# Kernel optimization log

Hardware: AMD Instinct MI355X
Metric: run time of the kernel (lower is better)

## Reference

```python
import jax, jax.numpy as jnp
import numpy as np

N_NODES = 8192
N_EDGES = 32768
D = 768
H1 = 8
NEG_SLOPE = 0.2


def setup_inputs() -> dict:
    key = jax.random.key(0)
    ks = jax.random.split(key, 10)
    s = 0.02  # init scale keeps attention logits numerically tame
    x = jax.random.normal(ks[0], (N_NODES, D), dtype=jnp.float32)
    edge_index = jax.random.randint(ks[1], (2, N_EDGES), 0, N_NODES, dtype=jnp.int64)
    W1 = jax.random.normal(ks[2], (D, H1 * D), dtype=jnp.float32) * s
    a_src1 = jax.random.normal(ks[3], (H1, D), dtype=jnp.float32) * s
    a_dst1 = jax.random.normal(ks[4], (H1, D), dtype=jnp.float32) * s
    b1 = jnp.zeros((H1 * D,), dtype=jnp.float32)
    W2 = jax.random.normal(ks[5], (H1 * D, D), dtype=jnp.float32) * s
    a_src2 = jax.random.normal(ks[6], (1, D), dtype=jnp.float32) * s
    a_dst2 = jax.random.normal(ks[7], (1, D), dtype=jnp.float32) * s
    b2 = jnp.zeros((D,), dtype=jnp.float32)
    return {"x": x, "edge_index": edge_index, "W1": W1, "a_src1": a_src1,
            "a_dst1": a_dst1, "b1": b1, "W2": W2, "a_src2": a_src2,
            "a_dst2": a_dst2, "b2": b2}


def gat_conv(x, src, dst, W, a_src, a_dst, b, heads, out_ch):
    """PyG GATConv (concat=True, self-loops already appended to src/dst)."""
    n = x.shape[0]
    h = (x @ W).reshape(n, heads, out_ch)            # [N,H,C]
    alpha_src = jnp.einsum("nhc,hc->nh", h, a_src)  # [N,H]
    alpha_dst = jnp.einsum("nhc,hc->nh", h, a_dst)  # [N,H]
    # edge scores: leaky_relu(a_src.h_j + a_dst.h_i) for edge j->i
    e = jax.nn.leaky_relu(alpha_src[src] + alpha_dst[dst], NEG_SLOPE)  # [E,H]
    # segment softmax over incoming edges of each destination node
    m = jax.ops.segment_max(e, dst, num_segments=n)   # [N,H]
    m = jnp.where(jnp.isfinite(m), m, 0.0)
    p = jnp.exp(e - m[dst])                           # [E,H]
    denom = jax.ops.segment_sum(p, dst, num_segments=n)
    alpha = p / denom[dst]                            # [E,H]
    msg = h[src] * alpha[:, :, None]                  # [E,H,C] gather+weight
    out = jax.ops.segment_sum(msg, dst, num_segments=n)  # [N,H,C] scatter-add
    return out.reshape(n, heads * out_ch) + b


def reference(x, edge_index, W1, a_src1, a_dst1, b1, W2, a_src2, a_dst2, b2):
    n = x.shape[0]
    loops = jnp.arange(n, dtype=edge_index.dtype)
    src = jnp.concatenate([edge_index[0], loops])  # add_self_loops=True
    dst = jnp.concatenate([edge_index[1], loops])
    h = gat_conv(x, src, dst, W1, a_src1, a_dst1, b1, H1, D)
    h = jax.nn.elu(h)
    out = gat_conv(h, src, dst, W2, a_src2, a_dst2, b2, 1, D)
    return out
```

## Files before the change

kernel.cpp:

```cpp
#include <hip/hip_runtime.h>
#include <hip/hip_bf16.h>


#define N_NODES 8192
#define N_EDGES 32768
#define E_TOT   (N_EDGES + N_NODES)
#define D_IN    768
#define H1      8
#define HC1     (H1 * D_IN)
#define KSPLIT  4
#define KSLICE  (HC1 / KSPLIT)

typedef unsigned short ushort_t;
using short8  = __attribute__((ext_vector_type(8))) short;
using floatx4 = __attribute__((ext_vector_type(4))) float;

__device__ __forceinline__ float bf2f(unsigned short u) {
  return __uint_as_float(((unsigned)u) << 16);
}
__device__ __forceinline__ unsigned short f2bf(float f) {
  unsigned u = __float_as_uint(f);
  unsigned r = (u + 0x7fffu + ((u >> 16) & 1u)) >> 16;
  return (unsigned short)r;
}

__device__ __forceinline__ void gll16(const ushort_t* g, ushort_t* l) {
  __builtin_amdgcn_global_load_lds(
      (const __attribute__((address_space(1))) void*)g,
      (__attribute__((address_space(3))) void*)l, 16, 0, 0);
}

__global__ __launch_bounds__(64) void frag_transpose_kernel(
    const float* __restrict__ W, ushort_t* __restrict__ out,
    int Kdim, int Ndim) {
  const int bn = blockIdx.x;
  const int bk = blockIdx.y;
  const int lane = threadIdx.x;
  const int lrow = lane & 15, lq = lane >> 4;
  const int n = bn * 16 + lrow;
  const int kb = bk * 32 + lq * 8;
  ushort_t v[8];
#pragma unroll
  for (int e = 0; e < 8; ++e)
    v[e] = f2bf(W[(size_t)(kb + e) * Ndim + n]);
  *(short8*)(out + ((size_t)bn * (Kdim >> 5) + bk) * 512 + lane * 8) =
      *(short8*)v;
}

__global__ void prep_aw_kernel(const float* __restrict__ W1,
                               const float* __restrict__ aS,
                               const float* __restrict__ aD,
                               float* __restrict__ awS,
                               float* __restrict__ awD) {
  const int d = blockIdx.x;
  const int t = threadIdx.x;
  const float* row = W1 + (size_t)d * HC1;
  float ps[H1], pd[H1];
#pragma unroll
  for (int h = 0; h < H1; ++h) { ps[h] = 0.f; pd[h] = 0.f; }
#pragma unroll
  for (int h = 0; h < H1; ++h)
#pragma unroll
    for (int j = 0; j < 3; ++j) {
      int idx = h * 768 + j * 256 + t;
      float w = row[idx];
      ps[h] += w * aS[idx];
      pd[h] += w * aD[idx];
    }
#pragma unroll
  for (int h = 0; h < H1; ++h)
    for (int off = 32; off > 0; off >>= 1) {
      ps[h] += __shfl_down(ps[h], off, 64);
      pd[h] += __shfl_down(pd[h], off, 64);
    }
  __shared__ float red[2][4][H1];
  int w = t >> 6;
  if ((t & 63) == 0) {
#pragma unroll
    for (int h = 0; h < H1; ++h) { red[0][w][h] = ps[h]; red[1][w][h] = pd[h]; }
  }
  __syncthreads();
  if (t < H1)
    awS[d * H1 + t] = red[0][0][t] + red[0][1][t] + red[0][2][t] + red[0][3][t];
  else if (t >= 64 && t < 64 + H1) {
    int h = t - 64;
    awD[d * H1 + h] = red[1][0][h] + red[1][1][h] + red[1][2][h] + red[1][3][h];
  }
}

__global__ void node_prep_kernel(const float* __restrict__ x,
                                 const float* __restrict__ awS,
                                 const float* __restrict__ awD,
                                 ushort_t* __restrict__ xb,
                                 float* __restrict__ as1,
                                 float* __restrict__ ad1) {
  const int n = blockIdx.x;
  const int t = threadIdx.x;
  float ps[H1], pd[H1];
#pragma unroll
  for (int h = 0; h < H1; ++h) { ps[h] = 0.f; pd[h] = 0.f; }
#pragma unroll
  for (int j = 0; j < 3; ++j) {
    int d = j * 256 + t;
    float xv = x[(size_t)n * 768 + d];
    xb[(size_t)n * 768 + d] = f2bf(xv);
    const float4* s4 = (const float4*)(awS + d * 8);
    const float4* d4 = (const float4*)(awD + d * 8);
    float4 a0 = s4[0], a1 = s4[1];
    float4 c0 = d4[0], c1 = d4[1];
    ps[0] += xv * a0.x; ps[1] += xv * a0.y; ps[2] += xv * a0.z; ps[3] += xv * a0.w;
    ps[4] += xv * a1.x; ps[5] += xv * a1.y; ps[6] += xv * a1.z; ps[7] += xv * a1.w;
    pd[0] += xv * c0.x; pd[1] += xv * c0.y; pd[2] += xv * c0.z; pd[3] += xv * c0.w;
    pd[4] += xv * c1.x; pd[5] += xv * c1.y; pd[6] += xv * c1.z; pd[7] += xv * c1.w;
  }
#pragma unroll
  for (int h = 0; h < H1; ++h)
    for (int off = 32; off > 0; off >>= 1) {
      ps[h] += __shfl_down(ps[h], off, 64);
      pd[h] += __shfl_down(pd[h], off, 64);
    }
  __shared__ float red[2][4][H1];
  int w = t >> 6;
  if ((t & 63) == 0) {
#pragma unroll
    for (int h = 0; h < H1; ++h) { red[0][w][h] = ps[h]; red[1][w][h] = pd[h]; }
  }
  __syncthreads();
  if (t < H1)
    as1[n * H1 + t] = red[0][0][t] + red[0][1][t] + red[0][2][t] + red[0][3][t];
  else if (t >= 64 && t < 64 + H1) {
    int h = t - 64;
    ad1[n * H1 + h] = red[1][0][h] + red[1][1][h] + red[1][2][h] + red[1][3][h];
  }
}

__global__ void deg_kernel(const int* __restrict__ dst, int* __restrict__ deg) {
  int e = blockIdx.x * blockDim.x + threadIdx.x;
  if (e >= E_TOT) return;
  int d = (e < N_EDGES) ? dst[e] : (e - N_EDGES);
  atomicAdd(&deg[d], 1);
}

__global__ void scan_kernel(const int* __restrict__ deg, int* __restrict__ start,
                            int* __restrict__ cursor) {
  __shared__ int sums[1024];
  int t = threadIdx.x;
  int base = t * 8;
  int local[8];
  int s = 0;
#pragma unroll
  for (int i = 0; i < 8; ++i) { local[i] = s; s += deg[base + i]; }
  sums[t] = s;
  __syncthreads();
  for (int off = 1; off < 1024; off <<= 1) {
    int v = (t >= off) ? sums[t - off] : 0;
    __syncthreads();
    sums[t] += v;
    __syncthreads();
  }
  int excl = (t == 0) ? 0 : sums[t - 1];
#pragma unroll
  for (int i = 0; i < 8; ++i) {
    int st = excl + local[i];
    start[base + i] = st;
    cursor[base + i] = st;
  }
}

__global__ void fill_kernel(const int* __restrict__ dst, int* __restrict__ cursor,
                            int* __restrict__ csr) {
  int e = blockIdx.x * blockDim.x + threadIdx.x;
  if (e >= E_TOT) return;
  int d = (e < N_EDGES) ? dst[e] : (e - N_EDGES);
  int pos = atomicAdd(&cursor[d], 1);
  csr[pos] = e;
}

__global__ __launch_bounds__(256) void attn1_kernel(
    const ushort_t* __restrict__ xb, const float* __restrict__ as1,
    const float* __restrict__ ad1, const int* __restrict__ start,
    const int* __restrict__ deg, const int* __restrict__ csr,
    const int* __restrict__ src, ushort_t* __restrict__ z_sw) {
  const int n = blockIdx.x;
  const int t = threadIdx.x;
  const int st = start[n], dg = deg[n];
  const int h = t & 7, eloc = t >> 3;
  __shared__ float invd[H1];
  __shared__ float alphaS[16][H1];
  __shared__ int sidx[16];
  __shared__ float red[4][H1];
  __shared__ uint4 xs[16 * 96];

  const float adv = ad1[n * H1 + h];
  float pden = 0.f;
  for (int base = 0; base < dg; base += 32) {
    int ei = base + eloc;
    if (ei < dg) {
      int e = csr[st + ei];
      int s = (e < N_EDGES) ? src[e] : (e - N_EDGES);
      float l = as1[s * H1 + h] + adv;
      l = l > 0.f ? l : 0.2f * l;
      pden += __expf(l);
    }
  }
  pden += __shfl_down(pden, 8, 64);
  pden += __shfl_down(pden, 16, 64);
  pden += __shfl_down(pden, 32, 64);
  if ((t & 63) < 8) red[t >> 6][h] = pden;
  __syncthreads();
  if (t < 8) invd[t] = 1.0f / (red[0][t] + red[1][t] + red[2][t] + red[3][t]);
  __syncthreads();

  int hp[3], ip[3];
#pragma unroll
  for (int p = 0; p < 3; ++p) {
    int c8 = p * 256 + t;
    hp[p] = c8 / 96;
    ip[p] = c8 % 96;
  }
  float acc[3][8];
#pragma unroll
  for (int p = 0; p < 3; ++p)
#pragma unroll
    for (int e = 0; e < 8; ++e) acc[p][e] = 0.f;

  for (int base = 0; base < dg; base += 16) {
    int cnt = dg - base; if (cnt > 16) cnt = 16;
    if (t < 128 && eloc < cnt) {
      int e = csr[st + base + eloc];
      int s = (e < N_EDGES) ? src[e] : (e - N_EDGES);
      float l = as1[s * H1 + h] + adv;
      l = l > 0.f ? l : 0.2f * l;
      alphaS[eloc][h] = __expf(l) * invd[h];
      if (h == 0) sidx[eloc] = s;
    }
    __syncthreads();
#pragma unroll
    for (int j = 0; j < 6; ++j) {
      int idx = t + 256 * j;
      int row = idx / 96;
      if (row < cnt) {
        int col = idx - row * 96;
        xs[idx] = *(const uint4*)(xb + (size_t)sidx[row] * 768 + col * 8);
      }
    }
    __syncthreads();
    for (int ei = 0; ei < cnt; ++ei) {
      const uint4* xr = &xs[ei * 96];
#pragma unroll
      for (int p = 0; p < 3; ++p) {
        uint4 v = xr[ip[p]];
        float al = alphaS[ei][hp[p]];
        unsigned uu[4] = {v.x, v.y, v.z, v.w};
#pragma unroll
        for (int q = 0; q < 4; ++q) {
          acc[p][2 * q]     += al * __uint_as_float(uu[q] << 16);
          acc[p][2 * q + 1] += al * __uint_as_float(uu[q] & 0xffff0000u);
        }
      }
    }
    __syncthreads();
  }
#pragma unroll
  for (int p = 0; p < 3; ++p) {
    int c8 = p * 256 + t;
    int k = c8 * 8;
    size_t chunk = (size_t)(n >> 4) * 192 + (k >> 5);
    int word = ((k >> 3) & 3) * 16 + (n & 15);
    ushort_t v[8];
#pragma unroll
    for (int e = 0; e < 8; ++e) v[e] = f2bf(acc[p][e]);
    *(short8*)(z_sw + chunk * 512 + word * 8) = *(short8*)v;
  }
}

#define STAGE_RING(t)                                                          \
  {                                                                            \
    ushort_t* ld_ = smem + ((t) & 3) * 16384 + slot512;                        \
    _Pragma("unroll") for (int q_ = 0; q_ < 4; ++q_)                           \
        gll16(SRC + (((size_t)(cb[q_] + (t))) << 9) + lane8, ld_ + q_ * 512);  \
  }

#define GSTEP_BODY(s, VMSTR, NSV)                                             \
  {                                                                           \
    asm volatile("s_waitcnt vmcnt(" VMSTR ")" ::: "memory");                  \
    __builtin_amdgcn_s_barrier();                                             \
    const ushort_t* buf_ = smem + ((s) & 3) * 16384;                          \
    short8 af[8], bf[4];                                                      \
    _Pragma("unroll") for (int j_ = 0; j_ < 4; ++j_)                          \
        bf[j_] = *(const short8*)(buf_ + 8192 + (wn * 4 + j_) * 512 + lane8); \
    _Pragma("unroll") for (int i_ = 0; i_ < 4; ++i_)                          \
        af[i_] = *(const short8*)(buf_ + (wm * 8 + i_) * 512 + lane8);        \
    if ((s) + 3 < (NSV)) STAGE_RING((s) + 3)                                  \
    __builtin_amdgcn_s_setprio(1);                                            \
    _Pragma("unroll") for (int i_ = 0; i_ < 4; ++i_)                          \
        _Pragma("unroll") for (int j_ = 0; j_ < 4; ++j_)                      \
            acc[i_][j_] = __builtin_amdgcn_mfma_f32_16x16x32_bf16(            \
                af[i_], bf[j_], acc[i_][j_], 0, 0, 0);                        \
    __builtin_amdgcn_s_setprio(0);                                            \
    _Pragma("unroll") for (int i_ = 4; i_ < 8; ++i_)                          \
        af[i_] = *(const short8*)(buf_ + (wm * 8 + i_) * 512 + lane8);        \
    __builtin_amdgcn_s_barrier();                                             \
    __builtin_amdgcn_s_setprio(1);                                            \
    _Pragma("unroll") for (int i_ = 4; i_ < 8; ++i_)                          \
        _Pragma("unroll") for (int j_ = 0; j_ < 4; ++j_)                      \
            acc[i_][j_] = __builtin_amdgcn_mfma_f32_16x16x32_bf16(            \
                af[i_], bf[j_], acc[i_][j_], 0, 0, 0);                        \
    __builtin_amdgcn_s_setprio(0);                                            \
  }

#define GEMM_PIPE(NSV)                                                        \
  _Pragma("unroll") for (int p_ = 0; p_ < 3; ++p_) STAGE_RING(p_)             \
  _Pragma("unroll 2") for (int s_ = 0; s_ < (NSV)-2; ++s_) {                  \
    GSTEP_BODY(s_, "8", (NSV))                                                \
  }                                                                           \
  GSTEP_BODY((NSV)-2, "4", (NSV))                                             \
  GSTEP_BODY((NSV)-1, "0", (NSV))

__global__ __launch_bounds__(512, 2) void gemm_l1_kernel(
    const ushort_t* __restrict__ Asw, const ushort_t* __restrict__ Bsw,
    const float* __restrict__ biasb, ushort_t* __restrict__ Csw) {
  __shared__ ushort_t smem[4 * 16384];
  const int id = blockIdx.x;
  const int head = id & 7;
  const int j_id = id >> 3;
  const int n_t = j_id % 3;
  const int m_t = j_id / 3;
  const int tid = threadIdx.x;
  const int lane = tid & 63;
  const int w = tid >> 6;
  const int wm = w >> 2, wn = w & 3;
  const int lrow = lane & 15, lq = lane >> 4;
  const int lane8 = lane * 8;
  const int slot512 = w * 2048;
  const ushort_t* SRC = (w < 4) ? Asw : Bsw;

  int cb[4];
#pragma unroll
  for (int q = 0; q < 4; ++q) {
    int v;
    if (w < 4)
      v = (m_t * 16 + 4 * w + q) * 192 + head * 24;
    else
      v = (head * 48 + n_t * 16 + 4 * (w - 4) + q) * 24;
    cb[q] = __builtin_amdgcn_readfirstlane(v);
  }

  floatx4 acc[8][4];
#pragma unroll
  for (int i = 0; i < 8; ++i)
#pragma unroll
    for (int j = 0; j < 4; ++j) acc[i][j] = {0.f, 0.f, 0.f, 0.f};

  GEMM_PIPE(24)

  __syncthreads();
  ushort_t* tile = smem;
  const float* bias = biasb + head * 768 + n_t * 256;
#pragma unroll
  for (int p = 0; p < 2; ++p) {
    if (p) __syncthreads();
    if (wm == p) {
#pragma unroll
      for (int i = 0; i < 8; ++i)
#pragma unroll
        for (int j = 0; j < 4; ++j) {
          int col = wn * 64 + j * 16 + lrow;
          float bv = bias[col];
#pragma unroll
          for (int r = 0; r < 4; ++r) {
            float v = acc[i][j][r] + bv;
            v = v > 0.f ? v : __expf(v) - 1.0f;
            tile[(i * 16 + lq * 4 + r) * 280 + col] = f2bf(v);
          }
        }
    }
    __syncthreads();
#pragma unroll
    for (int cc = 0; cc < 8; ++cc) {
      int ch = w * 8 + cc;
      int RB = ch >> 3, kg = ch & 7;
      short8 vv =
          *(const short8*)&tile[(RB * 16 + lrow) * 280 + kg * 32 + lq * 8];
      size_t chunk_g = (size_t)(m_t * 16 + p * 8 + RB) * 192 + head * 24 +
                       n_t * 8 + kg;
      *((short8*)Csw + chunk_g * 64 + lane) = vv;
    }
  }
}

__global__ __launch_bounds__(512, 2) void gemm_l2_kernel(
    const ushort_t* __restrict__ Asw, const ushort_t* __restrict__ Bsw,
    float* __restrict__ Cp) {
  __shared__ ushort_t smem[4 * 16384];
  const int id = blockIdx.x;
  const int c = id & 7;
  const int sl = c >> 1;
  const int j_id = id >> 3;
  const int n_t = j_id % 3;
  const int m_t = (j_id / 3) * 2 + (c & 1);
  const int tid = threadIdx.x;
  const int lane = tid & 63;
  const int w = tid >> 6;
  const int wm = w >> 2, wn = w & 3;
  const int lrow = lane & 15, lq = lane >> 4;
  const int lane8 = lane * 8;
  const int slot512 = w * 2048;
  const ushort_t* SRC = (w < 4) ? Asw : Bsw;

  int cb[4];
#pragma unroll
  for (int q = 0; q < 4; ++q) {
    int v;
    if (w < 4)
      v = (m_t * 16 + 4 * w + q) * 192 + sl * 48;
    else
      v = (n_t * 16 + 4 * (w - 4) + q) * 192 + sl * 48;
    cb[q] = __builtin_amdgcn_readfirstlane(v);
  }

  floatx4 acc[8][4];
#pragma unroll
  for (int i = 0; i < 8; ++i)
#pragma unroll
    for (int j = 0; j < 4; ++j) acc[i][j] = {0.f, 0.f, 0.f, 0.f};

  GEMM_PIPE(48)

  float* C = Cp + (size_t)sl * N_NODES * 768;
  const int m0 = m_t * 256, n0 = n_t * 256;
#pragma unroll
  for (int i = 0; i < 8; ++i) {
    int row_b = m0 + wm * 128 + i * 16 + lq * 4;
#pragma unroll
    for (int j = 0; j < 4; ++j) {
      int col = n0 + wn * 64 + j * 16 + lrow;
#pragma unroll
      for (int r = 0; r < 4; ++r)
        C[(size_t)(row_b + r) * 768 + col] = acc[i][j][r];
    }
  }
}

__global__ void reduce_alpha2_kernel(const float* __restrict__ parts,
                                     const float* __restrict__ aS,
                                     const float* __restrict__ aD,
                                     ushort_t* __restrict__ yb,
                                     float* __restrict__ as2,
                                     float* __restrict__ ad2) {
  const int n = blockIdx.x;
  const int t = threadIdx.x;
  const size_t S = (size_t)N_NODES * 768;
  float ps = 0.f, pd = 0.f;
#pragma unroll
  for (int j = 0; j < 3; ++j) {
    int cidx = j * 256 + t;
    size_t base = (size_t)n * 768 + cidx;
    float v = parts[base] + parts[base + S] + parts[base + 2 * S] +
              parts[base + 3 * S];
    yb[base] = f2bf(v);
    ps += v * aS[cidx];
    pd += v * aD[cidx];
  }
  for (int off = 32; off > 0; off >>= 1) {
    ps += __shfl_down(ps, off, 64);
    pd += __shfl_down(pd, off, 64);
  }
  __shared__ float red[2][4];
  int w = t >> 6;
  if ((t & 63) == 0) { red[0][w] = ps; red[1][w] = pd; }
  __syncthreads();
  if (t == 0) as2[n] = red[0][0] + red[0][1] + red[0][2] + red[0][3];
  if (t == 64) ad2[n] = red[1][0] + red[1][1] + red[1][2] + red[1][3];
}

__global__ __launch_bounds__(256) void attn2_kernel(
    const ushort_t* __restrict__ yb, const float* __restrict__ as2,
    const float* __restrict__ ad2, const int* __restrict__ start,
    const int* __restrict__ deg, const int* __restrict__ csr,
    const int* __restrict__ src, const float* __restrict__ b2,
    float* __restrict__ out) {
  const int n = blockIdx.x;
  const int t = threadIdx.x;
  const int st = start[n], dg = deg[n];
  __shared__ float alphaS[64];
  __shared__ int sidx[64];
  __shared__ float red[4];
  __shared__ float invd_sh;

  const float adv = ad2[n];
  float pden = 0.f;
  for (int ei = t; ei < dg; ei += 256) {
    int e = csr[st + ei];
    int s = (e < N_EDGES) ? src[e] : (e - N_EDGES);
    float l = as2[s] + adv;
    l = l > 0.f ? l : 0.2f * l;
    pden += __expf(l);
  }
  for (int off = 32; off > 0; off >>= 1) pden += __shfl_down(pden, off, 64);
  if ((t & 63) == 0) red[t >> 6] = pden;
  __syncthreads();
  if (t == 0) invd_sh = 1.0f / (red[0] + red[1] + red[2] + red[3]);
  __syncthreads();
  const float invd = invd_sh;

  float a0 = 0.f, a1 = 0.f, a2 = 0.f;
  for (int base = 0; base < dg; base += 64) {
    int cnt = dg - base; if (cnt > 64) cnt = 64;
    if (t < cnt) {
      int e = csr[st + base + t];
      int s = (e < N_EDGES) ? src[e] : (e - N_EDGES);
      float l = as2[s] + adv;
      l = l > 0.f ? l : 0.2f * l;
      alphaS[t] = __expf(l) * invd;
      sidx[t] = s;
    }
    __syncthreads();
    for (int ei = 0; ei < cnt; ++ei) {
      float al = alphaS[ei];
      const ushort_t* row = yb + (size_t)sidx[ei] * 768;
      a0 += al * bf2f(row[t]);
      a1 += al * bf2f(row[t + 256]);
      a2 += al * bf2f(row[t + 512]);
    }
    __syncthreads();
  }
  out[(size_t)n * 768 + t]       = a0 + b2[t];
  out[(size_t)n * 768 + t + 256] = a1 + b2[t + 256];
  out[(size_t)n * 768 + t + 512] = a2 + b2[t + 512];
}

extern "C" void kernel_launch(void* const* d_in, const int* in_sizes, int n_in,
                              void* d_out, int out_size, void* d_ws, size_t ws_size,
                              hipStream_t stream) {
  const float* x      = (const float*)d_in[0];
  const int*   ei     = (const int*)d_in[1];
  const float* W1     = (const float*)d_in[2];
  const float* a_src1 = (const float*)d_in[3];
  const float* a_dst1 = (const float*)d_in[4];
  const float* b1     = (const float*)d_in[5];
  const float* W2     = (const float*)d_in[6];
  const float* a_src2 = (const float*)d_in[7];
  const float* a_dst2 = (const float*)d_in[8];
  const float* b2     = (const float*)d_in[9];
  float* out = (float*)d_out;
  const int* src = ei;
  const int* dst = ei + N_EDGES;

  char* ws = (char*)d_ws;
  size_t off = 0;
  auto alloc = [&](size_t bytes) -> void* {
    void* p = ws + off;
    off = (off + bytes + 255) & ~(size_t)255;
    return p;
  };

  int* deg = (int*)alloc(N_NODES * 4);
  float* awS = (float*)alloc(768 * H1 * 4);
  float* awD = (float*)alloc(768 * H1 * 4);
  float* as1 = (float*)alloc(N_NODES * H1 * 4);
  float* ad1 = (float*)alloc(N_NODES * H1 * 4);
  float* as2 = (float*)alloc(N_NODES * 4);
  float* ad2 = (float*)alloc(N_NODES * 4);
  int* start  = (int*)alloc(N_NODES * 4);
  int* cursor = (int*)alloc(N_NODES * 4);
  int* csr    = (int*)alloc(E_TOT * 4);
  ushort_t* xb     = (ushort_t*)alloc((size_t)N_NODES * D_IN * 2);
  ushort_t* w1t_sw = (ushort_t*)alloc((size_t)HC1 * D_IN * 2 + 8192);
  ushort_t* w2t_sw = (ushort_t*)alloc((size_t)HC1 * D_IN * 2 + 8192);
  ushort_t* z_sw   = (ushort_t*)alloc((size_t)N_NODES * HC1 * 2 + 8192);
  ushort_t* h2b_sw = (ushort_t*)alloc((size_t)N_NODES * HC1 * 2 + 8192);
  ushort_t* yb  = xb;
  float* parts  = (float*)z_sw;
  (void)ws_size; (void)n_in; (void)in_sizes; (void)out_size;

  hipMemsetAsync(deg, 0, N_NODES * 4, stream);

  prep_aw_kernel<<<768, 256, 0, stream>>>(W1, a_src1, a_dst1, awS, awD);
  node_prep_kernel<<<N_NODES, 256, 0, stream>>>(x, awS, awD, xb, as1, ad1);
  frag_transpose_kernel<<<dim3(HC1 / 16, D_IN / 32), 64, 0, stream>>>(
      W1, w1t_sw, D_IN, HC1);
  frag_transpose_kernel<<<dim3(D_IN / 16, HC1 / 32), 64, 0, stream>>>(
      W2, w2t_sw, HC1, D_IN);

  deg_kernel<<<(E_TOT + 255) / 256, 256, 0, stream>>>(dst, deg);
  scan_kernel<<<1, 1024, 0, stream>>>(deg, start, cursor);
  fill_kernel<<<(E_TOT + 255) / 256, 256, 0, stream>>>(dst, cursor, csr);

  attn1_kernel<<<N_NODES, 256, 0, stream>>>(xb, as1, ad1, start, deg, csr,
                                            src, z_sw);
  gemm_l1_kernel<<<8 * 32 * 3, 512, 0, stream>>>(z_sw, w1t_sw, b1, h2b_sw);

  gemm_l2_kernel<<<KSPLIT * 2 * 16 * 3, 512, 0, stream>>>(h2b_sw, w2t_sw,
                                                          parts);
  reduce_alpha2_kernel<<<N_NODES, 256, 0, stream>>>(parts, a_src2, a_dst2, yb,
                                                    as2, ad2);
  attn2_kernel<<<N_NODES, 256, 0, stream>>>(yb, as2, ad2, start, deg, csr,
                                            src, b2, out);
}
```

Baseline: 462.6 us.

## Replace 4-slot K-step ring with double-buffered two-step tiles in GEMMs

Both GEMM kernels move from a 4-deep ring of single K-steps, with prefetch three ahead and partial vmcnt waits, to a 2-buffer scheme. Each buffer holds two K-steps, and each iteration prefetches the next tile while computing the current one. Interleaved LDS reads and MFMA clusters are separated by barriers, explicit lgkmcnt waits and sched_barriers. The aim is fewer barrier/wait points per K and a simpler schedule. The cost is shallower prefetch, since a full vmcnt(0) wait happens every tile, and there are more barriers inside each tile.

```diff
diff --git a/kernel.cpp b/kernel.cpp
--- a/kernel.cpp
+++ b/kernel.cpp
@@ -274,53 +274,66 @@
   }
 }
 
-#define STAGE_RING(t)                                                          \
-  {                                                                            \
-    ushort_t* ld_ = smem + ((t) & 3) * 16384 + slot512;                        \
-    _Pragma("unroll") for (int q_ = 0; q_ < 4; ++q_)                           \
-        gll16(SRC + (((size_t)(cb[q_] + (t))) << 9) + lane8, ld_ + q_ * 512);  \
-  }
-
-#define GSTEP_BODY(s, VMSTR, NSV)                                             \
+#define STAGE_TILE(t)                                                         \
   {                                                                           \
-    asm volatile("s_waitcnt vmcnt(" VMSTR ")" ::: "memory");                  \
+    ushort_t* ld_ = smem + ((t) & 1) * 32768 + slotu;                         \
+    _Pragma("unroll") for (int kk_ = 0; kk_ < 2; ++kk_)                       \
+      _Pragma("unroll") for (int q_ = 0; q_ < 4; ++q_)                        \
+        gll16(SRC + (((size_t)(cb[q_] + 2 * (t) + kk_)) << 9) + lane8,        \
+              ld_ + kk_ * 16384 + q_ * 512);                                  \
+  }
+
+#define READS_A(tb_, kk)                                                      \
+    _Pragma("unroll") for (int j_ = 0; j_ < 4; ++j_)                          \
+      bf[j_] = *(const short8*)((tb_) + (kk) * 16384 + 8192 +                 \
+                                (wn * 4 + j_) * 512 + lane8);                 \
+    _Pragma("unroll") for (int i_ = 0; i_ < 4; ++i_)                          \
+      af[i_] = *(const short8*)((tb_) + (kk) * 16384 +                        \
+                                (wm * 8 + i_) * 512 + lane8);
+
+#define READS_B(tb_, kk)                                                      \
+    _Pragma("unroll") for (int i_ = 0; i_ < 4; ++i_)                          \
+      af2[i_] = *(const short8*)((tb_) + (kk) * 16384 +                       \
+                                 (wm * 8 + 4 + i_) * 512 + lane8);
+
+#define MFMA_CL(ab, FR)                                                       \
     __builtin_amdgcn_s_barrier();                                             \
-    const ushort_t* buf_ = smem + ((s) & 3) * 16384;                          \
-    short8 af[8], bf[4];                                                      \
-    _Pragma("unroll") for (int j_ = 0; j_ < 4; ++j_)                          \
-        bf[j_] = *(const short8*)(buf_ + 8192 + (wn * 4 + j_) * 512 + lane8); \
-    _Pragma("unroll") for (int i_ = 0; i_ < 4; ++i_)                          \
-        af[i_] = *(const short8*)(buf_ + (wm * 8 + i_) * 512 + lane8);        \
-    if ((s) + 3 < (NSV)) STAGE_RING((s) + 3)                                  \
+    asm volatile("s_waitcnt lgkmcnt(0)" ::: "memory");                        \
+    __builtin_amdgcn_sched_barrier(0);                                        \
     __builtin_amdgcn_s_setprio(1);                                            \
     _Pragma("unroll") for (int i_ = 0; i_ < 4; ++i_)                          \
-        _Pragma("unroll") for (int j_ = 0; j_ < 4; ++j_)                      \
-            acc[i_][j_] = __builtin_amdgcn_mfma_f32_16x16x32_bf16(            \
-                af[i_], bf[j_], acc[i_][j_], 0, 0, 0);                        \
-    __builtin_amdgcn_s_setprio(0);                                            \
-    _Pragma("unroll") for (int i_ = 4; i_ < 8; ++i_)                          \
-        af[i_] = *(const short8*)(buf_ + (wm * 8 + i_) * 512 + lane8);        \
+      _Pragma("unroll") for (int j_ = 0; j_ < 4; ++j_)                        \
+        acc[(ab) + i_][j_] = __builtin_amdgcn_mfma_f32_16x16x32_bf16(         \
+            FR[i_], bf[j_], acc[(ab) + i_][j_], 0, 0, 0);                     \
+    __builtin_amdgcn_s_setprio(0);
+
+#define GEMM_TILE8(t, NT)                                                     \
+  {                                                                           \
+    asm volatile("s_waitcnt vmcnt(0)" ::: "memory");                          \
     __builtin_amdgcn_s_barrier();                                             \
-    __builtin_amdgcn_s_setprio(1);                                            \
-    _Pragma("unroll") for (int i_ = 4; i_ < 8; ++i_)                          \
-        _Pragma("unroll") for (int j_ = 0; j_ < 4; ++j_)                      \
-            acc[i_][j_] = __builtin_amdgcn_mfma_f32_16x16x32_bf16(            \
-                af[i_], bf[j_], acc[i_][j_], 0, 0, 0);                        \
-    __builtin_amdgcn_s_setprio(0);                                            \
-  }
-
-#define GEMM_PIPE(NSV)                                                        \
-  _Pragma("unroll") for (int p_ = 0; p_ < 3; ++p_) STAGE_RING(p_)             \
-  _Pragma("unroll 2") for (int s_ = 0; s_ < (NSV)-2; ++s_) {                  \
-    GSTEP_BODY(s_, "8", (NSV))                                                \
-  }                                                                           \
-  GSTEP_BODY((NSV)-2, "4", (NSV))                                             \
-  GSTEP_BODY((NSV)-1, "0", (NSV))
+    if ((t) + 1 < (NT)) STAGE_TILE((t) + 1)                                   \
+    const ushort_t* tb_ = smem + ((t) & 1) * 32768;                           \
+    short8 af[4], af2[4], bf[4];                                              \
+    READS_A(tb_, 0)                                                           \
+    MFMA_CL(0, af)                                                            \
+    READS_B(tb_, 0)                                                           \
+    MFMA_CL(4, af2)                                                           \
+    READS_A(tb_, 1)                                                           \
+    MFMA_CL(0, af)                                                            \
+    READS_B(tb_, 1)                                                           \
+    MFMA_CL(4, af2)                                                           \
+  }
+
+#define GEMM_PIPE8(NT)                                                        \
+  STAGE_TILE(0)                                                               \
+  _Pragma("unroll 2") for (int t_ = 0; t_ < (NT); ++t_) {                     \
+    GEMM_TILE8(t_, (NT))                                                      \
+  }
 
 __global__ __launch_bounds__(512, 2) void gemm_l1_kernel(
     const ushort_t* __restrict__ Asw, const ushort_t* __restrict__ Bsw,
     const float* __restrict__ biasb, ushort_t* __restrict__ Csw) {
-  __shared__ ushort_t smem[4 * 16384];
+  __shared__ ushort_t smem[65536];
   const int id = blockIdx.x;
   const int head = id & 7;
   const int j_id = id >> 3;
@@ -332,7 +345,7 @@
   const int wm = w >> 2, wn = w & 3;
   const int lrow = lane & 15, lq = lane >> 4;
   const int lane8 = lane * 8;
-  const int slot512 = w * 2048;
+  const int slotu = (w < 4) ? w * 2048 : 8192 + (w - 4) * 2048;
   const ushort_t* SRC = (w < 4) ? Asw : Bsw;
 
   int cb[4];
@@ -352,7 +365,7 @@
 #pragma unroll
     for (int j = 0; j < 4; ++j) acc[i][j] = {0.f, 0.f, 0.f, 0.f};
 
-  GEMM_PIPE(24)
+  GEMM_PIPE8(12)
 
   __syncthreads();
   ushort_t* tile = smem;
@@ -392,7 +405,7 @@
 __global__ __launch_bounds__(512, 2) void gemm_l2_kernel(
     const ushort_t* __restrict__ Asw, const ushort_t* __restrict__ Bsw,
     float* __restrict__ Cp) {
-  __shared__ ushort_t smem[4 * 16384];
+  __shared__ ushort_t smem[65536];
   const int id = blockIdx.x;
   const int c = id & 7;
   const int sl = c >> 1;
@@ -405,7 +418,7 @@
   const int wm = w >> 2, wn = w & 3;
   const int lrow = lane & 15, lq = lane >> 4;
   const int lane8 = lane * 8;
-  const int slot512 = w * 2048;
+  const int slotu = (w < 4) ? w * 2048 : 8192 + (w - 4) * 2048;
   const ushort_t* SRC = (w < 4) ? Asw : Bsw;
 
   int cb[4];
@@ -425,7 +438,7 @@
 #pragma unroll
     for (int j = 0; j < 4; ++j) acc[i][j] = {0.f, 0.f, 0.f, 0.f};
 
-  GEMM_PIPE(48)
+  GEMM_PIPE8(24)
 
   float* C = Cp + (size_t)sl * N_NODES * 768;
   const int m0 = m_t * 256, n0 = n_t * 256;
```

Result: slower. 475.1 us (+2.7%).

## Fuse W1 attention-weight precompute into LDS-tiled bf16 fragment transpose

Applied to the files above, without the earlier changes.

The weight transpose kernels now stage a 64x64 fp32 tile in padded LDS so global reads are coalesced, then emit the bf16 MFMA fragment layout from shared memory. The separate prep_aw pass over W1 is folded into the W1 transpose. It reuses the staged tile to compute the per-head a_src/a_dst projections and accumulates them with atomics, so it needs two extra memsets. This drops a full re-read of W1 and the strided uncoalesced loads of the old transpose, at the cost of atomic float accumulation with nondeterministic summation order.

```diff
diff --git a/kernel.cpp b/kernel.cpp
--- a/kernel.cpp
+++ b/kernel.cpp
@@ -30,61 +30,84 @@
       (__attribute__((address_space(3))) void*)l, 16, 0, 0);
 }
 
-__global__ __launch_bounds__(64) void frag_transpose_kernel(
+__global__ __launch_bounds__(256) void frag_transpose_kernel(
     const float* __restrict__ W, ushort_t* __restrict__ out,
     int Kdim, int Ndim) {
-  const int bn = blockIdx.x;
-  const int bk = blockIdx.y;
-  const int lane = threadIdx.x;
-  const int lrow = lane & 15, lq = lane >> 4;
-  const int n = bn * 16 + lrow;
-  const int kb = bk * 32 + lq * 8;
-  ushort_t v[8];
-#pragma unroll
-  for (int e = 0; e < 8; ++e)
-    v[e] = f2bf(W[(size_t)(kb + e) * Ndim + n]);
-  *(short8*)(out + ((size_t)bn * (Kdim >> 5) + bk) * 512 + lane * 8) =
-      *(short8*)v;
-}
-
-__global__ void prep_aw_kernel(const float* __restrict__ W1,
-                               const float* __restrict__ aS,
-                               const float* __restrict__ aD,
-                               float* __restrict__ awS,
-                               float* __restrict__ awD) {
-  const int d = blockIdx.x;
-  const int t = threadIdx.x;
-  const float* row = W1 + (size_t)d * HC1;
-  float ps[H1], pd[H1];
-#pragma unroll
-  for (int h = 0; h < H1; ++h) { ps[h] = 0.f; pd[h] = 0.f; }
-#pragma unroll
-  for (int h = 0; h < H1; ++h)
-#pragma unroll
-    for (int j = 0; j < 3; ++j) {
-      int idx = h * 768 + j * 256 + t;
-      float w = row[idx];
-      ps[h] += w * aS[idx];
-      pd[h] += w * aD[idx];
-    }
-#pragma unroll
-  for (int h = 0; h < H1; ++h)
-    for (int off = 32; off > 0; off >>= 1) {
-      ps[h] += __shfl_down(ps[h], off, 64);
-      pd[h] += __shfl_down(pd[h], off, 64);
-    }
-  __shared__ float red[2][4][H1];
-  int w = t >> 6;
-  if ((t & 63) == 0) {
-#pragma unroll
-    for (int h = 0; h < H1; ++h) { red[0][w][h] = ps[h]; red[1][w][h] = pd[h]; }
-  }
-  __syncthreads();
-  if (t < H1)
-    awS[d * H1 + t] = red[0][0][t] + red[0][1][t] + red[0][2][t] + red[0][3][t];
-  else if (t >= 64 && t < 64 + H1) {
-    int h = t - 64;
-    awD[d * H1 + h] = red[1][0][h] + red[1][1][h] + red[1][2][h] + red[1][3][h];
+  __shared__ float lds[64 * 65];
+  const int bx = blockIdx.x;
+  const int by = blockIdx.y;
+  const int tid = threadIdx.x;
+  const int n0 = bx * 64, k0 = by * 64;
+  const int nn = tid & 63, kq = tid >> 6;
+#pragma unroll
+  for (int it = 0; it < 16; ++it) {
+    int kk = it * 4 + kq;
+    lds[kk * 65 + nn] = W[(size_t)(k0 + kk) * Ndim + n0 + nn];
+  }
+  __syncthreads();
+  const int Ksub = Kdim >> 5;
+#pragma unroll
+  for (int it = 0; it < 2; ++it) {
+    int idx = tid + 256 * it;
+    int c = idx >> 6, l = idx & 63;
+    int cn = c >> 1, ck = c & 1;
+    int lrow = l & 15, lq = l >> 4;
+    int n_loc = cn * 16 + lrow;
+    int kb = ck * 32 + lq * 8;
+    ushort_t v[8];
+#pragma unroll
+    for (int e = 0; e < 8; ++e) v[e] = f2bf(lds[(kb + e) * 65 + n_loc]);
+    size_t chunk = (size_t)(bx * 4 + cn) * Ksub + (by * 2 + ck);
+    *(short8*)(out + chunk * 512 + l * 8) = *(short8*)v;
+  }
+}
+
+__global__ __launch_bounds__(256) void frag_transpose_aw_kernel(
+    const float* __restrict__ W, ushort_t* __restrict__ out,
+    const float* __restrict__ aS, const float* __restrict__ aD,
+    float* __restrict__ awS, float* __restrict__ awD) {
+  __shared__ float lds[64 * 65];
+  const int bx = blockIdx.x;
+  const int by = blockIdx.y;
+  const int tid = threadIdx.x;
+  const int n0 = bx * 64, k0 = by * 64;
+  const int nn = tid & 63, kq = tid >> 6;
+#pragma unroll
+  for (int it = 0; it < 16; ++it) {
+    int kk = it * 4 + kq;
+    lds[kk * 65 + nn] = W[(size_t)(k0 + kk) * 6144 + n0 + nn];
+  }
+  __syncthreads();
+#pragma unroll
+  for (int it = 0; it < 2; ++it) {
+    int idx = tid + 256 * it;
+    int c = idx >> 6, l = idx & 63;
+    int cn = c >> 1, ck = c & 1;
+    int lrow = l & 15, lq = l >> 4;
+    int n_loc = cn * 16 + lrow;
+    int kb = ck * 32 + lq * 8;
+    ushort_t v[8];
+#pragma unroll
+    for (int e = 0; e < 8; ++e) v[e] = f2bf(lds[(kb + e) * 65 + n_loc]);
+    size_t chunk = (size_t)(bx * 4 + cn) * 24 + (by * 2 + ck);
+    *(short8*)(out + chunk * 512 + l * 8) = *(short8*)v;
+  }
+  const int r = tid >> 2, nq = tid & 3;
+  float s_ = 0.f, d_ = 0.f;
+  const float* aSp = aS + n0 + nq * 16;
+  const float* aDp = aD + n0 + nq * 16;
+#pragma unroll
+  for (int c = 0; c < 16; ++c) {
+    float v = lds[r * 65 + nq * 16 + c];
+    s_ += v * aSp[c];
+    d_ += v * aDp[c];
+  }
+  s_ += __shfl_down(s_, 2, 4); s_ += __shfl_down(s_, 1, 4);
+  d_ += __shfl_down(d_, 2, 4); d_ += __shfl_down(d_, 1, 4);
+  if (nq == 0) {
+    int h = n0 / 768;
+    atomicAdd(&awS[(k0 + r) * H1 + h], s_);
+    atomicAdd(&awD[(k0 + r) * H1 + h], d_);
   }
 }
 
@@ -575,13 +598,14 @@
   (void)ws_size; (void)n_in; (void)in_sizes; (void)out_size;
 
   hipMemsetAsync(deg, 0, N_NODES * 4, stream);
-
-  prep_aw_kernel<<<768, 256, 0, stream>>>(W1, a_src1, a_dst1, awS, awD);
+  hipMemsetAsync(awS, 0, 768 * H1 * 4, stream);
+  hipMemsetAsync(awD, 0, 768 * H1 * 4, stream);
+
+  frag_transpose_aw_kernel<<<dim3(HC1 / 64, D_IN / 64), 256, 0, stream>>>(
+      W1, w1t_sw, a_src1, a_dst1, awS, awD);
+  frag_transpose_kernel<<<dim3(D_IN / 64, HC1 / 64), 256, 0, stream>>>(
+      W2, w2t_sw, HC1, D_IN);
   node_prep_kernel<<<N_NODES, 256, 0, stream>>>(x, awS, awD, xb, as1, ad1);
-  frag_transpose_kernel<<<dim3(HC1 / 16, D_IN / 32), 64, 0, stream>>>(
-      W1, w1t_sw, D_IN, HC1);
-  frag_transpose_kernel<<<dim3(D_IN / 16, HC1 / 32), 64, 0, stream>>>(
-      W2, w2t_sw, HC1, D_IN);
 
   deg_kernel<<<(E_TOT + 255) / 256, 256, 0, stream>>>(dst, deg);
   scan_kernel<<<1, 1024, 0, stream>>>(deg, start, cursor);
```

New measurement: 462.1 us. Within noise of the previous version (-0.1%).
